# Performance work log

Measured on AMD Instinct MI355X. Metric: run time of the kernel, lower is better.

## Reference

```python
import jax, jax.numpy as jnp
import numpy as np

HEADS = 8
DIM_HEAD = 64
NB_FEATURES = 266
EPS = 1e-4


def softmax_kernel(data, projection, is_query):
    # data: (b, h, n, d); projection: (m, d)
    dn = data.shape[-1] ** -0.25                       # data normalizer d^{-1/4}
    ratio = projection.shape[0] ** -0.5                # m^{-1/2}
    dd = jnp.einsum('bhnd,md->bhnm', dn * data, projection)
    diag = (jnp.sum(data * data, axis=-1, keepdims=True) * 0.5) * (dn * dn)
    stab = jnp.max(dd, axis=-1, keepdims=True) if is_query else jnp.max(dd)
    return ratio * (jnp.exp(dd - diag - stab) + EPS)


def linear_attention(q, k, v):
    # q,k: (b,h,n,m) kernel features; v: (b,h,n,d)
    k_sum = k.sum(axis=-2)                                   # (b,h,m)
    D_inv = 1.0 / jnp.einsum('bhnm,bhm->bhn', q, k_sum)      # (b,h,n)
    context = jnp.einsum('bhnm,bhnd->bhmd', k, v)            # (b,h,m,d)
    return jnp.einsum('bhmd,bhnm,bhn->bhnd', context, q, D_inv)


def reference(x, W_qkv, W_out, projection, f):
    B, N, dim = x.shape
    h, dh = HEADS, DIM_HEAD
    qkv = x @ W_qkv                                          # (B,N,3*h*dh)
    q, k, v = jnp.split(qkv, 3, axis=-1)
    to_bh = lambda t: t.reshape(B, N, h, dh).transpose(0, 2, 1, 3).reshape(B * h, N, dh)
    q, k, v = to_bh(q), to_bh(k), to_bh(v)
    q = q * (dh ** -0.5)
    cls_q, q_ = q[:, :1], q[:, 1:]
    cls_k, k_ = k[:, :1], k[:, 1:]
    cls_v, v_ = v[:, :1], v[:, 1:]
    # cls token attends to ALL tokens with exact softmax attention
    sim = jnp.einsum('bid,bjd->bij', cls_q, k)
    cls_out = jnp.einsum('bij,bjd->bid', jax.nn.softmax(sim, axis=-1), v)
    # space attention regroup: 'b (f n) d -> (b f) n d'
    n_sp = (N - 1) // f
    grp = lambda t: t.reshape(B * h * f, n_sp, dh)
    q_, k_, v_ = grp(q_), grp(k_), grp(v_)
    # broadcast cls k/v to each group: 'b () d -> (b r) () d', r = f
    k_ = jnp.concatenate([jnp.repeat(cls_k, f, axis=0), k_], axis=1)  # (B*h*f, n_sp+1, dh)
    v_ = jnp.concatenate([jnp.repeat(cls_v, f, axis=0), v_], axis=1)
    # '(b h) f d -> b h f d'
    sh = lambda t: t.reshape(-1, h, t.shape[1], dh)
    qp = softmax_kernel(sh(q_), projection, True)
    kp = softmax_kernel(sh(k_), projection, False)
    out = linear_attention(qp, kp, sh(v_))                   # (-1, h, n_sp, dh)
    out = out.reshape(B * h, f * n_sp, dh)                   # '(b f) n d -> b (f n) d'
    out = jnp.concatenate([cls_out, out], axis=1)            # (B*h, N, dh)
    out = out.reshape(B, h, N, dh).transpose(0, 2, 1, 3).reshape(B, N, h * dh)
    return out @ W_out


def setup_inputs():
    key = jax.random.key(0)
    ks = jax.random.split(key, 3)
    B, F, S, dim = 8, 16, 196, 512
    N = 1 + F * S
    dh, m = DIM_HEAD, NB_FEATURES
    x = jax.random.normal(ks[0], (B, N, dim), dtype=jnp.float32)
    W_qkv = jax.random.normal(ks[1], (dim, 3 * dim), dtype=jnp.float32) * (dim ** -0.5)
    W_out = jax.random.normal(ks[2], (dim, dim), dtype=jnp.float32) * (dim ** -0.5)
    # gaussian orthogonal random matrix (scaling=0): QR blocks, chi-norm row scales
    rng = np.random.default_rng(0)
    blocks = []
    for _ in range(m // dh):
        qm, _ = np.linalg.qr(rng.standard_normal((dh, dh)))
        blocks.append(qm.T)
    rem = m - (m // dh) * dh
    if rem > 0:
        qm, _ = np.linalg.qr(rng.standard_normal((dh, dh)))
        blocks.append(qm.T[:rem])
    proj = np.concatenate(blocks, axis=0)
    multiplier = np.linalg.norm(rng.standard_normal((m, dh)), axis=1)
    projection = jnp.asarray(multiplier[:, None] * proj, dtype=jnp.float32)
    return {"x": x, "W_qkv": W_qkv, "W_out": W_out, "projection": projection, "f": F}
```

## Files before the change

kernel.cpp:

```cpp
#include <hip/hip_runtime.h>
#include <hip/hip_bf16.h>

namespace {

typedef __bf16 bf16x8 __attribute__((ext_vector_type(8)));
typedef float  f32x4  __attribute__((ext_vector_type(4)));
typedef unsigned short ushort8 __attribute__((ext_vector_type(8)));
typedef unsigned int u32;

constexpr int NTOK  = 3137;
constexpr int NH    = 8;
constexpr int DH    = 64;
constexpr int BH    = 64;
constexpr int MROWS = 8 * NTOK;
constexpr int NROWS = BH * NTOK;
constexpr int MF    = 266;
constexpr int MPK   = 320;
constexpr int MC    = 288;
constexpr int MS    = 320;
constexpr int NMAXB = (NROWS + 255) / 256;
constexpr int NCH   = 13;
constexpr int NBQKV = 197 * 12;
constexpr int NBOUT = 197 * 4;

constexpr float DN     = 0.35355339059327379f;
constexpr float HDN2   = 0.0625f;
constexpr float RATIO  = 0.0613139368f;
constexpr float EPSV   = 1.0e-4f;
constexpr float QSCALE = 0.125f;

__device__ __forceinline__ int swz64(int r, int c)  { return (r << 6) + (c ^ ((r & 7) << 3)); }
__device__ __forceinline__ int swz320(int r, int c) { return r * 320 + (c ^ ((r & 7) << 3)); }

__device__ __forceinline__ int xcdchunk(int bid, int nb) {
  const int q = nb >> 3, r = nb & 7;
  const int xcd = bid & 7, slot = bid >> 3;
  return (xcd < r ? xcd * (q + 1) : r * (q + 1) + (xcd - r) * q) + slot;
}

__device__ __forceinline__ float b2f(unsigned short u) {
  union { unsigned int i; float f; } cv;
  cv.i = ((unsigned int)u) << 16;
  return cv.f;
}
__device__ __forceinline__ unsigned short f2b(float f) {
  __hip_bfloat16 h = __float2bfloat16(f);
  union { __hip_bfloat16 h; unsigned short u; } cv;
  cv.h = h;
  return cv.u;
}
__device__ __forceinline__ unsigned int pk2(float a, float b) {
  return (unsigned int)f2b(a) | ((unsigned int)f2b(b) << 16);
}
__device__ __forceinline__ u32 fenc(float f) {
  u32 u = __float_as_uint(f);
  return (u & 0x80000000u) ? ~u : (u | 0x80000000u);
}
__device__ __forceinline__ float fdec(u32 u) {
  return __uint_as_float((u & 0x80000000u) ? (u ^ 0x80000000u) : ~u);
}
__device__ __forceinline__ void gload16(const void* g, void* l) {
  __builtin_amdgcn_global_load_lds(
      (const __attribute__((address_space(1))) u32*)g,
      (__attribute__((address_space(3))) u32*)l, 16, 0, 0);
}

__global__ __launch_bounds__(256) void k_projb(
    const float* __restrict__ proj, unsigned short* __restrict__ projb,
    u32* __restrict__ gmaxu)
{
  const int idx = (blockIdx.x * 256 + threadIdx.x) * 8;
  if (idx < MPK * 64) {
    const int m = idx >> 6, c0 = idx & 63;
    uint4 u;
    if (m < MF) {
      const float* src = proj + (size_t)m * 64 + c0;
      const float4 f0 = *(const float4*)src;
      const float4 f1 = *(const float4*)(src + 4);
      u.x = pk2(f0.x, f0.y); u.y = pk2(f0.z, f0.w);
      u.z = pk2(f1.x, f1.y); u.w = pk2(f1.z, f1.w);
    } else {
      u = uint4{0, 0, 0, 0};
    }
    *(uint4*)&projb[swz64(m, c0)] = u;
  }
  if (blockIdx.x == 0 && threadIdx.x == 0) *gmaxu = 0u;
}

__global__ __launch_bounds__(256) void k_cvt(
    const float* __restrict__ src, unsigned short* __restrict__ dst, int n8)
{
  const int i = blockIdx.x * 256 + threadIdx.x;
  if (i < n8) {
    const float4 f0 = *(const float4*)(src + (size_t)i * 8);
    const float4 f1 = *(const float4*)(src + (size_t)i * 8 + 4);
    uint4 u;
    u.x = pk2(f0.x, f0.y); u.y = pk2(f0.z, f0.w);
    u.z = pk2(f1.x, f1.y); u.w = pk2(f1.z, f1.w);
    *(uint4*)(dst + (size_t)i * 8) = u;
  }
}

__global__ __launch_bounds__(256) void k_tconv(
    const float* __restrict__ src, unsigned short* __restrict__ dst,
    int R, int C)
{
  __shared__ float tile[64][65];
  const int cb = blockIdx.x * 64, rb = blockIdx.y * 64;
  const int tid = threadIdx.x;
  const int tr = tid >> 4, tc4 = (tid & 15) * 4;
  #pragma unroll
  for (int i = 0; i < 4; ++i) {
    const int r = tr + i * 16;
    const float4 f = *(const float4*)(src + (size_t)(rb + r) * C + cb + tc4);
    tile[r][tc4 + 0] = f.x; tile[r][tc4 + 1] = f.y;
    tile[r][tc4 + 2] = f.z; tile[r][tc4 + 3] = f.w;
  }
  __syncthreads();
  #pragma unroll
  for (int i = 0; i < 4; ++i) {
    const int wrow = tr + i * 16;
    uint2 u;
    u.x = pk2(tile[tc4 + 0][wrow], tile[tc4 + 1][wrow]);
    u.y = pk2(tile[tc4 + 2][wrow], tile[tc4 + 3][wrow]);
    *(uint2*)&dst[(size_t)(cb + wrow) * R + rb + tc4] = u;
  }
}

__global__ __launch_bounds__(256) void k_qkv(
    const unsigned short* __restrict__ xb,
    const unsigned short* __restrict__ wT,
    unsigned short* __restrict__ qb, unsigned short* __restrict__ kb,
    unsigned short* __restrict__ vb)
{
  __shared__ alignas(16) unsigned short As[128 * 64];
  __shared__ alignas(16) unsigned short Bs[128 * 64];
  const int lid = xcdchunk(blockIdx.x, NBQKV);
  const int bm = lid / 12, bn = lid % 12;
  const int tid = threadIdx.x;
  const int lane = tid & 63, wid = tid >> 6;
  const int wr = wid >> 1, wc = wid & 1;
  const int row0 = bm * 128, col0 = bn * 128;
  const int l15 = lane & 15, l4 = lane >> 4;
  const int lr = lane >> 3;
  const int srcChunk = (lane & 7) ^ lr;

  const unsigned short* aRow[4];
  const unsigned short* bRow[4];
  #pragma unroll
  for (int j = 0; j < 4; ++j) {
    int gr = row0 + wid * 32 + j * 8 + lr;
    if (gr >= MROWS) gr = MROWS - 1;
    aRow[j] = xb + (size_t)gr * 512 + srcChunk * 8;
    bRow[j] = wT + (size_t)(col0 + wid * 32 + j * 8 + lr) * 512 + srcChunk * 8;
  }

  f32x4 acc[4][4];
  #pragma unroll
  for (int i = 0; i < 4; ++i)
    #pragma unroll
    for (int j = 0; j < 4; ++j) acc[i][j] = f32x4{0.f, 0.f, 0.f, 0.f};

  for (int kt = 0; kt < 512; kt += 64) {
    #pragma unroll
    for (int j = 0; j < 4; ++j) {
      gload16(aRow[j] + kt, &As[(wid * 32 + j * 8) * 64]);
      gload16(bRow[j] + kt, &Bs[(wid * 32 + j * 8) * 64]);
    }
    __syncthreads();
    #pragma unroll
    for (int ks = 0; ks < 2; ++ks) {
      bf16x8 af[4], bfr[4];
      #pragma unroll
      for (int i = 0; i < 4; ++i)
        af[i] = *(const bf16x8*)&As[swz64(wr * 64 + i * 16 + l15, ks * 32 + l4 * 8)];
      #pragma unroll
      for (int i = 0; i < 4; ++i)
        bfr[i] = *(const bf16x8*)&Bs[swz64(wc * 64 + i * 16 + l15, ks * 32 + l4 * 8)];
      #pragma unroll
      for (int mi = 0; mi < 4; ++mi)
        #pragma unroll
        for (int ni = 0; ni < 4; ++ni)
          acc[mi][ni] = __builtin_amdgcn_mfma_f32_16x16x32_bf16(
              af[mi], bfr[ni], acc[mi][ni], 0, 0, 0);
    }
    __syncthreads();
  }
  #pragma unroll
  for (int mi = 0; mi < 4; ++mi) {
    #pragma unroll
    for (int r = 0; r < 4; ++r) {
      const int grow = row0 + wr * 64 + mi * 16 + l4 * 4 + r;
      if (grow < MROWS) {
        const int bb = grow / NTOK, n = grow - bb * NTOK;
        #pragma unroll
        for (int ni = 0; ni < 4; ++ni) {
          const int gc = col0 + wc * 64 + ni * 16 + l15;
          const int which = gc >> 9;
          const int col = gc & 511;
          const int hh = col >> 6, d = col & 63;
          const size_t off = (size_t)((bb * NH + hh) * NTOK + n) * DH + d;
          const float vv = acc[mi][ni][r];
          if (which == 0)      qb[off] = f2b(vv * QSCALE);
          else if (which == 1) kb[off] = f2b(vv);
          else                 vb[off] = f2b(vv);
        }
      }
    }
  }
}

__global__ __launch_bounds__(256) void k_out(
    const unsigned short* __restrict__ a,
    const unsigned short* __restrict__ wT,
    float* __restrict__ out)
{
  __shared__ alignas(16) unsigned short As[128 * 64];
  __shared__ alignas(16) unsigned short Bs[128 * 64];
  const int lid = xcdchunk(blockIdx.x, NBOUT);
  const int bm = lid / 4, bn = lid % 4;
  const int tid = threadIdx.x;
  const int lane = tid & 63, wid = tid >> 6;
  const int wr = wid >> 1, wc = wid & 1;
  const int row0 = bm * 128, col0 = bn * 128;
  const int l15 = lane & 15, l4 = lane >> 4;
  const int lr = lane >> 3;
  const int srcChunk = (lane & 7) ^ lr;

  const unsigned short* aRow[4];
  const unsigned short* bRow[4];
  #pragma unroll
  for (int j = 0; j < 4; ++j) {
    int gr = row0 + wid * 32 + j * 8 + lr;
    if (gr >= MROWS) gr = MROWS - 1;
    aRow[j] = a + (size_t)gr * 512 + srcChunk * 8;
    bRow[j] = wT + (size_t)(col0 + wid * 32 + j * 8 + lr) * 512 + srcChunk * 8;
  }

  f32x4 acc[4][4];
  #pragma unroll
  for (int i = 0; i < 4; ++i)
    #pragma unroll
    for (int j = 0; j < 4; ++j) acc[i][j] = f32x4{0.f, 0.f, 0.f, 0.f};

  for (int kt = 0; kt < 512; kt += 64) {
    #pragma unroll
    for (int j = 0; j < 4; ++j) {
      gload16(aRow[j] + kt, &As[(wid * 32 + j * 8) * 64]);
      gload16(bRow[j] + kt, &Bs[(wid * 32 + j * 8) * 64]);
    }
    __syncthreads();
    #pragma unroll
    for (int ks = 0; ks < 2; ++ks) {
      bf16x8 af[4], bfr[4];
      #pragma unroll
      for (int i = 0; i < 4; ++i)
        af[i] = *(const bf16x8*)&As[swz64(wr * 64 + i * 16 + l15, ks * 32 + l4 * 8)];
      #pragma unroll
      for (int i = 0; i < 4; ++i)
        bfr[i] = *(const bf16x8*)&Bs[swz64(wc * 64 + i * 16 + l15, ks * 32 + l4 * 8)];
      #pragma unroll
      for (int mi = 0; mi < 4; ++mi)
        #pragma unroll
        for (int ni = 0; ni < 4; ++ni)
          acc[mi][ni] = __builtin_amdgcn_mfma_f32_16x16x32_bf16(
              af[mi], bfr[ni], acc[mi][ni], 0, 0, 0);
    }
    __syncthreads();
  }
  #pragma unroll
  for (int mi = 0; mi < 4; ++mi) {
    #pragma unroll
    for (int r = 0; r < 4; ++r) {
      const int grow = row0 + wr * 64 + mi * 16 + l4 * 4 + r;
      if (grow < MROWS) {
        #pragma unroll
        for (int ni = 0; ni < 4; ++ni) {
          const int gc = col0 + wc * 64 + ni * 16 + l15;
          out[(size_t)grow * 512 + gc] = acc[mi][ni][r];
        }
      }
    }
  }
}

__global__ __launch_bounds__(256) void k_cls1(
    const unsigned short* __restrict__ qb, const unsigned short* __restrict__ kb,
    float* __restrict__ simb, float* __restrict__ cmax)
{
  __shared__ float qv[64];
  __shared__ float sred[4];
  const int bh = blockIdx.x, ch = blockIdx.y, tid = threadIdx.x;
  if (tid < 64) qv[tid] = b2f(qb[(size_t)bh * NTOK * 64 + tid]);
  __syncthreads();
  const int j = ch * 256 + tid;
  float dot = -3e38f;
  if (j < NTOK) {
    const unsigned short* kr = kb + (size_t)bh * NTOK * 64 + (size_t)j * 64;
    dot = 0.f;
    #pragma unroll
    for (int d0 = 0; d0 < 64; d0 += 8) {
      const bf16x8 kv = *(const bf16x8*)(kr + d0);
      #pragma unroll
      for (int j2 = 0; j2 < 8; ++j2) dot += qv[d0 + j2] * (float)kv[j2];
    }
    simb[bh * 3200 + j] = dot;
  }
  float lm = dot;
  #pragma unroll
  for (int off = 32; off; off >>= 1) lm = fmaxf(lm, __shfl_xor(lm, off));
  if ((tid & 63) == 0) sred[tid >> 6] = lm;
  __syncthreads();
  if (tid == 0)
    cmax[bh * NCH + ch] = fmaxf(fmaxf(sred[0], sred[1]), fmaxf(sred[2], sred[3]));
}

__global__ __launch_bounds__(256) void k_cls2(
    const unsigned short* __restrict__ vb, const float* __restrict__ simb,
    const float* __restrict__ cmax, float* __restrict__ pacc,
    float* __restrict__ psum)
{
  __shared__ float pa[4][64];
  __shared__ float pw[4];
  const int bh = blockIdx.x, ch = blockIdx.y, tid = threadIdx.x;
  const int wave = tid >> 6, d = tid & 63;
  float mx = -3e38f;
  #pragma unroll
  for (int i = 0; i < NCH; ++i) mx = fmaxf(mx, cmax[bh * NCH + i]);
  float acc = 0.f, ps = 0.f;
  const int j0 = ch * 256 + wave * 64;
  for (int i = 0; i < 64; ++i) {
    const int j = j0 + i;
    if (j < NTOK) {
      const float p = __expf(simb[bh * 3200 + j] - mx);
      acc += p * b2f(vb[(size_t)bh * NTOK * 64 + (size_t)j * 64 + d]);
      ps += p;
    }
  }
  pa[wave][d] = acc;
  if (d == 0) pw[wave] = ps;
  __syncthreads();
  if (tid < 64)
    pacc[((size_t)bh * NCH + ch) * 64 + tid] = pa[0][tid] + pa[1][tid] + pa[2][tid] + pa[3][tid];
  if (tid == 0)
    psum[bh * NCH + ch] = pw[0] + pw[1] + pw[2] + pw[3];
}

__global__ __launch_bounds__(64) void k_cls3(
    const float* __restrict__ pacc, const float* __restrict__ psum,
    unsigned short* __restrict__ attnb)
{
  const int bh = blockIdx.x, d = threadIdx.x;
  float a = 0.f, s = 0.f;
  #pragma unroll
  for (int ch = 0; ch < NCH; ++ch) {
    a += pacc[((size_t)bh * NCH + ch) * 64 + d];
    s += psum[bh * NCH + ch];
  }
  const int bb = bh >> 3, hh = bh & 7;
  attnb[((size_t)bb * NTOK + 0) * 512 + hh * 64 + d] = f2b(a / s);
}

__global__ __launch_bounds__(256) void k_keymax(
    const unsigned short* __restrict__ kb, const unsigned short* __restrict__ projb,
    u32* __restrict__ gmaxu)
{
  __shared__ alignas(16) unsigned short projL[MPK * 64];
  __shared__ float red[4];
  const int blk = blockIdx.x, tid = threadIdx.x;
  const int lane = tid & 63, wave = tid >> 6;
  const int l15 = lane & 15, l4 = lane >> 4;
  const int mw0 = wave * 80;
  {
    const char* srcb = (const char*)projb;
    char* dstb = (char*)projL;
    #pragma unroll
    for (int j = 0; j < 10; ++j) {
      const int off = (j * 4 + wave) * 1024;
      gload16(srcb + off + lane * 16, dstb + off);
    }
  }
  __syncthreads();
  float lm = -3e38f;
  for (int rg = 0; rg < 4; ++rg) {
    const int row0 = (blk * 4 + rg) * 64;
    if (row0 >= NROWS) break;
    bf16x8 bfrag[4][2];
    #pragma unroll
    for (int tf = 0; tf < 4; ++tf) {
      int gr = row0 + tf * 16 + l15;
      if (gr >= NROWS) gr = NROWS - 1;
      #pragma unroll
      for (int ks = 0; ks < 2; ++ks)
        bfrag[tf][ks] = *(const bf16x8*)(kb + (size_t)gr * 64 + ks * 32 + l4 * 8);
    }
    f32x4 acc[5][4];
    #pragma unroll
    for (int i = 0; i < 5; ++i)
      #pragma unroll
      for (int j = 0; j < 4; ++j) acc[i][j] = f32x4{0.f, 0.f, 0.f, 0.f};
    #pragma unroll
    for (int mf = 0; mf < 5; ++mf) {
      const bf16x8 a0 = *(const bf16x8*)&projL[swz64(mw0 + mf * 16 + l15, l4 * 8)];
      const bf16x8 a1 = *(const bf16x8*)&projL[swz64(mw0 + mf * 16 + l15, 32 + l4 * 8)];
      #pragma unroll
      for (int tf = 0; tf < 4; ++tf) {
        acc[mf][tf] = __builtin_amdgcn_mfma_f32_16x16x32_bf16(a0, bfrag[tf][0], acc[mf][tf], 0, 0, 0);
        acc[mf][tf] = __builtin_amdgcn_mfma_f32_16x16x32_bf16(a1, bfrag[tf][1], acc[mf][tf], 0, 0, 0);
      }
    }
    #pragma unroll
    for (int tf = 0; tf < 4; ++tf) {
      const bool colok = (row0 + tf * 16 + l15) < NROWS;
      #pragma unroll
      for (int mf = 0; mf < 5; ++mf)
        #pragma unroll
        for (int r = 0; r < 4; ++r) {
          const int m = mw0 + mf * 16 + l4 * 4 + r;
          if (colok && m < MF) lm = fmaxf(lm, DN * acc[mf][tf][r]);
        }
    }
  }
  #pragma unroll
  for (int off = 32; off; off >>= 1) lm = fmaxf(lm, __shfl_xor(lm, off));
  if (lane == 0) red[wave] = lm;
  __syncthreads();
  if (tid == 0) {
    const float bm = fmaxf(fmaxf(red[0], red[1]), fmaxf(red[2], red[3]));
    atomicMax(gmaxu, fenc(bm));
  }
}

__global__ __launch_bounds__(512) void k_ctx(
    const unsigned short* __restrict__ kb, const unsigned short* __restrict__ vb,
    const unsigned short* __restrict__ projb, const u32* __restrict__ gmaxu,
    unsigned short* __restrict__ ctxg, float* __restrict__ ksumg)
{
  __shared__ alignas(16) unsigned short kpT[MC * 64];
  __shared__ alignas(16) unsigned short vT[64 * 64];
  __shared__ float diag_l[64];

  const int g = blockIdx.x, bh = g >> 4, c = g & 15;
  const int tid = threadIdx.x;
  const int lane = tid & 63, wave = tid >> 6;
  const int l15 = lane & 15, l4 = lane >> 4;
  const int nf = (wave < 2) ? 3 : 2;
  const int M0 = (wave < 2) ? wave * 48 : 96 + (wave - 2) * 32;
  const float gm = fdec(*gmaxu);

  bf16x8 pfr[3][2];
  #pragma unroll
  for (int mf = 0; mf < 3; ++mf)
    #pragma unroll
    for (int ks = 0; ks < 2; ++ks)
      pfr[mf][ks] = (mf < nf)
          ? *(const bf16x8*)&projb[swz64(M0 + mf * 16 + l15, ks * 32 + l4 * 8)]
          : bf16x8{0, 0, 0, 0, 0, 0, 0, 0};

  const unsigned short* ksrc = kb + (size_t)bh * NTOK * 64;
  const unsigned short* vsrc = vb + (size_t)bh * NTOK * 64;

  f32x4 ctxacc[3][4];
  #pragma unroll
  for (int i = 0; i < 3; ++i)
    #pragma unroll
    for (int j = 0; j < 4; ++j) ctxacc[i][j] = f32x4{0.f, 0.f, 0.f, 0.f};
  float ksump[3][4];
  #pragma unroll
  for (int i = 0; i < 3; ++i)
    #pragma unroll
    for (int j = 0; j < 4; ++j) ksump[i][j] = 0.f;

  for (int kt = 0; kt < 4; ++kt) {
    __syncthreads();
    {
      const int t = tid & 63, dblk = (tid >> 6) & 7;
      const int n = kt * 64 + t;
      if (n < 197) {
        const int node = (n == 0) ? 0 : 1 + c * 196 + (n - 1);
        const ushort8 v = *(const ushort8*)(vsrc + (size_t)node * 64 + dblk * 8);
        #pragma unroll
        for (int j = 0; j < 8; ++j) vT[swz64(dblk * 8 + j, t)] = v[j];
      } else {
        #pragma unroll
        for (int j = 0; j < 8; ++j) vT[swz64(dblk * 8 + j, t)] = 0;
      }
    }
    if (tid < 64) {
      const int n = kt * 64 + tid;
      const int nn = (n < 197) ? n : 0;
      const int node = (nn == 0) ? 0 : 1 + c * 196 + (nn - 1);
      const unsigned short* kr = ksrc + (size_t)node * 64;
      float s = 0.f;
      #pragma unroll
      for (int d0 = 0; d0 < 64; d0 += 8) {
        const bf16x8 v = *(const bf16x8*)(kr + d0);
        #pragma unroll
        for (int j = 0; j < 8; ++j) { const float f = (float)v[j]; s += f * f; }
      }
      diag_l[tid] = HDN2 * s;
    }
    __syncthreads();
    #pragma unroll
    for (int tf = 0; tf < 4; ++tf) {
      const int n = kt * 64 + tf * 16 + l15;
      const int nn = (n < 197) ? n : 0;
      const int node = (nn == 0) ? 0 : 1 + c * 196 + (nn - 1);
      bf16x8 b0 = *(const bf16x8*)(ksrc + (size_t)node * 64 + l4 * 8);
      bf16x8 b1 = *(const bf16x8*)(ksrc + (size_t)node * 64 + 32 + l4 * 8);
      f32x4 a1[3];
      #pragma unroll
      for (int mf = 0; mf < 3; ++mf) {
        a1[mf] = f32x4{0.f, 0.f, 0.f, 0.f};
        if (mf < nf) {
          a1[mf] = __builtin_amdgcn_mfma_f32_16x16x32_bf16(pfr[mf][0], b0, a1[mf], 0, 0, 0);
          a1[mf] = __builtin_amdgcn_mfma_f32_16x16x32_bf16(pfr[mf][1], b1, a1[mf], 0, 0, 0);
        }
      }
      const int t = tf * 16 + l15;
      const int nv = kt * 64 + t;
      const float dg = diag_l[t];
      #pragma unroll
      for (int mf = 0; mf < 3; ++mf) {
        if (mf < nf) {
          #pragma unroll
          for (int r = 0; r < 4; ++r) {
            const int m = M0 + mf * 16 + l4 * 4 + r;
            float kp = 0.f;
            if (m < MF && nv < 197)
              kp = RATIO * (__expf(DN * a1[mf][r] - dg - gm) + EPSV);
            ksump[mf][r] += kp;
            kpT[swz64(m, t)] = f2b(kp);
          }
        }
      }
    }
    #pragma unroll
    for (int ks = 0; ks < 2; ++ks) {
      bf16x8 a2[3];
      #pragma unroll
      for (int mf = 0; mf < 3; ++mf)
        if (mf < nf)
          a2[mf] = *(const bf16x8*)&kpT[swz64(M0 + mf * 16 + l15, ks * 32 + l4 * 8)];
      #pragma unroll
      for (int df = 0; df < 4; ++df) {
        const bf16x8 b2 = *(const bf16x8*)&vT[swz64(df * 16 + l15, ks * 32 + l4 * 8)];
        #pragma unroll
        for (int mf = 0; mf < 3; ++mf)
          if (mf < nf)
            ctxacc[mf][df] = __builtin_amdgcn_mfma_f32_16x16x32_bf16(a2[mf], b2, ctxacc[mf][df], 0, 0, 0);
      }
    }
  }
  #pragma unroll
  for (int mf = 0; mf < 3; ++mf) {
    if (mf < nf) {
      #pragma unroll
      for (int r = 0; r < 4; ++r) {
        float v = ksump[mf][r];
        v += __shfl_xor(v, 1); v += __shfl_xor(v, 2);
        v += __shfl_xor(v, 4); v += __shfl_xor(v, 8);
        if (l15 == 0) ksumg[(size_t)g * MC + M0 + mf * 16 + l4 * 4 + r] = v;
      }
    }
  }
  #pragma unroll
  for (int mf = 0; mf < 3; ++mf) {
    if (mf < nf) {
      #pragma unroll
      for (int df = 0; df < 4; ++df) {
        const int d = df * 16 + l15;
        const int m = M0 + mf * 16 + l4 * 4;
        uint2 u;
        u.x = pk2(ctxacc[mf][df][0], ctxacc[mf][df][1]);
        u.y = pk2(ctxacc[mf][df][2], ctxacc[mf][df][3]);
        *(uint2*)&ctxg[(size_t)g * 64 * MS + swz320(d, m)] = u;
      }
    }
  }
}

__global__ __launch_bounds__(512) void k_qry(
    const unsigned short* __restrict__ qb, const unsigned short* __restrict__ projb,
    const unsigned short* __restrict__ ctxg, const float* __restrict__ ksumg,
    unsigned short* __restrict__ attnb)
{
  __shared__ alignas(16) unsigned short qp[64 * 320];
  __shared__ alignas(16) unsigned short ctxL[64 * 320];
  __shared__ float diag_l[64];
  __shared__ float rmax_l[8][64];
  __shared__ float dnm_l[8][64];

  const int g = blockIdx.x, bh = g >> 4, c = g & 15;
  const int bb = bh >> 3, hh = bh & 7;
  const int tid = threadIdx.x;
  const int lane = tid & 63, wave = tid >> 6;
  const int l15 = lane & 15, l4 = lane >> 4;
  const int nf = (wave < 2) ? 3 : 2;
  const int M0 = (wave < 2) ? wave * 48 : 96 + (wave - 2) * 32;

  {
    const char* srcb = (const char*)(ctxg + (size_t)g * 64 * MS);
    char* dstb = (char*)ctxL;
    #pragma unroll
    for (int j = 0; j < 5; ++j) {
      const int off = (j * 8 + wave) * 1024;
      gload16(srcb + off + lane * 16, dstb + off);
    }
  }

  bf16x8 pfr[3][2];
  #pragma unroll
  for (int mf = 0; mf < 3; ++mf)
    #pragma unroll
    for (int ks = 0; ks < 2; ++ks)
      pfr[mf][ks] = (mf < nf)
          ? *(const bf16x8*)&projb[swz64(M0 + mf * 16 + l15, ks * 32 + l4 * 8)]
          : bf16x8{0, 0, 0, 0, 0, 0, 0, 0};

  float ksr[3][4];
  #pragma unroll
  for (int mf = 0; mf < 3; ++mf) {
    if (mf < nf) {
      const float4 kv = *(const float4*)(ksumg + (size_t)g * MC + M0 + mf * 16 + l4 * 4);
      ksr[mf][0] = kv.x; ksr[mf][1] = kv.y; ksr[mf][2] = kv.z; ksr[mf][3] = kv.w;
    } else {
      ksr[mf][0] = ksr[mf][1] = ksr[mf][2] = ksr[mf][3] = 0.f;
    }
  }

  const unsigned short* qsrc = qb + (size_t)bh * NTOK * 64;
  const int tf4 = wave & 3, dfh = wave >> 2;

  for (int qt = 0; qt < 4; ++qt) {
    __syncthreads();
    if (tid < 64) {
      const int n = qt * 64 + tid;
      const int nn = (n < 196) ? n : 0;
      const int node = 1 + c * 196 + nn;
      const unsigned short* qr = qsrc + (size_t)node * 64;
      float s = 0.f;
      #pragma unroll
      for (int d0 = 0; d0 < 64; d0 += 8) {
        const bf16x8 v = *(const bf16x8*)(qr + d0);
        #pragma unroll
        for (int j = 0; j < 8; ++j) { const float f = (float)v[j]; s += f * f; }
      }
      diag_l[tid] = HDN2 * s;
    }
    f32x4 acc3[3][4];
    #pragma unroll
    for (int i = 0; i < 3; ++i)
      #pragma unroll
      for (int j = 0; j < 4; ++j) acc3[i][j] = f32x4{0.f, 0.f, 0.f, 0.f};
    #pragma unroll
    for (int tf = 0; tf < 4; ++tf) {
      const int n = qt * 64 + tf * 16 + l15;
      const int nn = (n < 196) ? n : 0;
      const int node = 1 + c * 196 + nn;
      bf16x8 b0 = *(const bf16x8*)(qsrc + (size_t)node * 64 + l4 * 8);
      bf16x8 b1 = *(const bf16x8*)(qsrc + (size_t)node * 64 + 32 + l4 * 8);
      #pragma unroll
      for (int mf = 0; mf < 3; ++mf) {
        if (mf < nf) {
          acc3[mf][tf] = __builtin_amdgcn_mfma_f32_16x16x32_bf16(pfr[mf][0], b0, acc3[mf][tf], 0, 0, 0);
          acc3[mf][tf] = __builtin_amdgcn_mfma_f32_16x16x32_bf16(pfr[mf][1], b1, acc3[mf][tf], 0, 0, 0);
        }
      }
    }
    #pragma unroll
    for (int tf = 0; tf < 4; ++tf) {
      float v = -3e38f;
      #pragma unroll
      for (int mf = 0; mf < 3; ++mf)
        if (mf < nf)
          #pragma unroll
          for (int r = 0; r < 4; ++r) {
            const int m = M0 + mf * 16 + l4 * 4 + r;
            if (m < MF) v = fmaxf(v, DN * acc3[mf][tf][r]);
          }
      v = fmaxf(v, __shfl_xor(v, 16));
      v = fmaxf(v, __shfl_xor(v, 32));
      if (l4 == 0) rmax_l[wave][tf * 16 + l15] = v;
    }
    __syncthreads();
    #pragma unroll
    for (int tf = 0; tf < 4; ++tf) {
      const int t = tf * 16 + l15;
      const int tq = qt * 64 + t;
      float rm = fmaxf(fmaxf(rmax_l[0][t], rmax_l[1][t]), fmaxf(rmax_l[2][t], rmax_l[3][t]));
      rm = fmaxf(rm, fmaxf(fmaxf(rmax_l[4][t], rmax_l[5][t]), fmaxf(rmax_l[6][t], rmax_l[7][t])));
      const float dg = diag_l[t];
      float dpart = 0.f;
      #pragma unroll
      for (int mf = 0; mf < 3; ++mf) {
        if (mf < nf) {
          float e[4];
          #pragma unroll
          for (int r = 0; r < 4; ++r) {
            const int m = M0 + mf * 16 + l4 * 4 + r;
            e[r] = (m < MF && tq < 196)
                 ? RATIO * (__expf(DN * acc3[mf][tf][r] - dg - rm) + EPSV) : 0.f;
            dpart += e[r] * ksr[mf][r];
          }
          uint2 u; u.x = pk2(e[0], e[1]); u.y = pk2(e[2], e[3]);
          *(uint2*)&qp[swz320(t, M0 + mf * 16 + l4 * 4)] = u;
        }
      }
      dpart += __shfl_xor(dpart, 16);
      dpart += __shfl_xor(dpart, 32);
      if (l4 == 0) dnm_l[wave][t] = dpart;
    }
    __syncthreads();
    f32x4 oacc[2];
    oacc[0] = f32x4{0.f, 0.f, 0.f, 0.f};
    oacc[1] = f32x4{0.f, 0.f, 0.f, 0.f};
    #pragma unroll
    for (int ks = 0; ks < 9; ++ks) {
      const bf16x8 a4 = *(const bf16x8*)&qp[swz320(tf4 * 16 + l15, ks * 32 + l4 * 8)];
      #pragma unroll
      for (int di = 0; di < 2; ++di) {
        const int d = dfh * 32 + di * 16 + l15;
        const bf16x8 b4 = *(const bf16x8*)&ctxL[swz320(d, ks * 32 + l4 * 8)];
        oacc[di] = __builtin_amdgcn_mfma_f32_16x16x32_bf16(a4, b4, oacc[di], 0, 0, 0);
      }
    }
    #pragma unroll
    for (int r = 0; r < 4; ++r) {
      const int tl = tf4 * 16 + l4 * 4 + r;
      const int tq = qt * 64 + tl;
      if (tq < 196) {
        float denom = 0.f;
        #pragma unroll
        for (int w8 = 0; w8 < 8; ++w8) denom += dnm_l[w8][tl];
        const float dinv = 1.0f / denom;
        const int node = 1 + c * 196 + tq;
        unsigned short* orow = attnb + ((size_t)bb * NTOK + node) * 512 + hh * 64 + dfh * 32;
        #pragma unroll
        for (int di = 0; di < 2; ++di)
          orow[di * 16 + l15] = f2b(oacc[di][r] * dinv);
      }
    }
  }
}

}

extern "C" void kernel_launch(void* const* d_in, const int* in_sizes, int n_in,
                              void* d_out, int out_size, void* d_ws, size_t ws_size,
                              hipStream_t stream) {
  (void)in_sizes; (void)n_in; (void)out_size; (void)ws_size;
  const float* x    = (const float*)d_in[0];
  const float* wqkv = (const float*)d_in[1];
  const float* wout = (const float*)d_in[2];
  const float* proj = (const float*)d_in[3];
  float* out = (float*)d_out;

  const size_t QKV = (size_t)BH * NTOK * DH;
  unsigned short* qb    = (unsigned short*)d_ws;
  unsigned short* kb    = qb + QKV;
  unsigned short* vb    = kb + QKV;
  unsigned short* attnb = vb + QKV;
  float* fbase = (float*)(attnb + QKV);
  u32*   gmaxu = (u32*)(fbase + 4096);
  float* simb = fbase + 8192;
  float* cmax = simb + 64 * 3200;
  float* pacc = cmax + 1024;
  float* psum = pacc + 64 * NCH * 64;
  unsigned short* wqkvT = (unsigned short*)(psum + 1024);
  unsigned short* woutT = wqkvT + 1536 * 512;
  unsigned short* ctxg  = woutT + 512 * 512;
  float* ksumg = (float*)(ctxg + (size_t)1024 * 64 * MS);
  unsigned short* projb = (unsigned short*)(ksumg + 1024 * MC);
  unsigned short* xb = attnb;

  const dim3 blk(256);
  k_projb  <<<dim3(10),       blk, 0, stream>>>(proj, projb, gmaxu);
  k_tconv  <<<dim3(24, 8),    blk, 0, stream>>>(wqkv, wqkvT, 512, 1536);
  k_tconv  <<<dim3(8, 8),     blk, 0, stream>>>(wout, woutT, 512, 512);
  k_cvt    <<<dim3((int)(QKV / 8 + 255) / 256), blk, 0, stream>>>(x, xb, (int)(QKV / 8));
  k_qkv    <<<dim3(NBQKV),    blk, 0, stream>>>(xb, wqkvT, qb, kb, vb);
  k_cls1   <<<dim3(BH, NCH),  blk, 0, stream>>>(qb, kb, simb, cmax);
  k_cls2   <<<dim3(BH, NCH),  blk, 0, stream>>>(vb, simb, cmax, pacc, psum);
  k_cls3   <<<dim3(BH), dim3(64), 0, stream>>>(pacc, psum, attnb);
  k_keymax <<<dim3(NMAXB),    blk, 0, stream>>>(kb, projb, gmaxu);
  k_ctx    <<<dim3(1024), dim3(512), 0, stream>>>(kb, vb, projb, gmaxu, ctxg, ksumg);
  k_qry    <<<dim3(1024), dim3(512), 0, stream>>>(qb, projb, ctxg, ksumg, attnb);
  k_out    <<<dim3(NBOUT),    blk, 0, stream>>>(attnb, woutT, out);
}
```

Baseline: 354.8 us.

## Software-pipeline query tiles in k_qry with double-buffered LDS

Splits the per-tile query loop into stages (diag, feature MFMA plus row max, exp/qp write, output MFMA). The output MFMA for the previous tile now runs alongside the feature MFMA for the current tile, using double-buffered qp, diag, rmax and dnm arrays in LDS. This removes one barrier per iteration and lets the two matrix phases interleave. In exchange the kernel uses roughly 40KB more LDS, which may reduce how many blocks fit on each CU.

```diff
diff --git a/kernel.cpp b/kernel.cpp
--- a/kernel.cpp
+++ b/kernel.cpp
@@ -585,11 +585,11 @@
     const unsigned short* __restrict__ ctxg, const float* __restrict__ ksumg,
     unsigned short* __restrict__ attnb)
 {
-  __shared__ alignas(16) unsigned short qp[64 * 320];
+  __shared__ alignas(16) unsigned short qp[2][64 * 320];
   __shared__ alignas(16) unsigned short ctxL[64 * 320];
-  __shared__ float diag_l[64];
-  __shared__ float rmax_l[8][64];
-  __shared__ float dnm_l[8][64];
+  __shared__ float diag_l[2][64];
+  __shared__ float rmax_l[2][8][64];
+  __shared__ float dnm_l[2][8][64];
 
   const int g = blockIdx.x, bh = g >> 4, c = g & 15;
   const int bb = bh >> 3, hh = bh & 7;
@@ -632,8 +632,7 @@
   const unsigned short* qsrc = qb + (size_t)bh * NTOK * 64;
   const int tf4 = wave & 3, dfh = wave >> 2;
 
-  for (int qt = 0; qt < 4; ++qt) {
-    __syncthreads();
+  auto diagf = [&](int qt, int buf) {
     if (tid < 64) {
       const int n = qt * 64 + tid;
       const int nn = (n < 196) ? n : 0;
@@ -646,9 +645,10 @@
         #pragma unroll
         for (int j = 0; j < 8; ++j) { const float f = (float)v[j]; s += f * f; }
       }
-      diag_l[tid] = HDN2 * s;
-    }
-    f32x4 acc3[3][4];
+      diag_l[buf][tid] = HDN2 * s;
+    }
+  };
+  auto stage3f = [&](int qt, int buf, f32x4 (&acc3)[3][4]) {
     #pragma unroll
     for (int i = 0; i < 3; ++i)
       #pragma unroll
@@ -681,16 +681,19 @@
           }
       v = fmaxf(v, __shfl_xor(v, 16));
       v = fmaxf(v, __shfl_xor(v, 32));
-      if (l4 == 0) rmax_l[wave][tf * 16 + l15] = v;
-    }
-    __syncthreads();
+      if (l4 == 0) rmax_l[buf][wave][tf * 16 + l15] = v;
+    }
+  };
+  auto qpwritef = [&](int qt, int buf, const f32x4 (&acc3)[3][4]) {
     #pragma unroll
     for (int tf = 0; tf < 4; ++tf) {
       const int t = tf * 16 + l15;
       const int tq = qt * 64 + t;
-      float rm = fmaxf(fmaxf(rmax_l[0][t], rmax_l[1][t]), fmaxf(rmax_l[2][t], rmax_l[3][t]));
-      rm = fmaxf(rm, fmaxf(fmaxf(rmax_l[4][t], rmax_l[5][t]), fmaxf(rmax_l[6][t], rmax_l[7][t])));
-      const float dg = diag_l[t];
+      float rm = fmaxf(fmaxf(rmax_l[buf][0][t], rmax_l[buf][1][t]),
+                       fmaxf(rmax_l[buf][2][t], rmax_l[buf][3][t]));
+      rm = fmaxf(rm, fmaxf(fmaxf(rmax_l[buf][4][t], rmax_l[buf][5][t]),
+                           fmaxf(rmax_l[buf][6][t], rmax_l[buf][7][t])));
+      const float dg = diag_l[buf][t];
       float dpart = 0.f;
       #pragma unroll
       for (int mf = 0; mf < 3; ++mf) {
@@ -704,20 +707,21 @@
             dpart += e[r] * ksr[mf][r];
           }
           uint2 u; u.x = pk2(e[0], e[1]); u.y = pk2(e[2], e[3]);
-          *(uint2*)&qp[swz320(t, M0 + mf * 16 + l4 * 4)] = u;
+          *(uint2*)&qp[buf][swz320(t, M0 + mf * 16 + l4 * 4)] = u;
         }
       }
       dpart += __shfl_xor(dpart, 16);
       dpart += __shfl_xor(dpart, 32);
-      if (l4 == 0) dnm_l[wave][t] = dpart;
-    }
-    __syncthreads();
+      if (l4 == 0) dnm_l[buf][wave][t] = dpart;
+    }
+  };
+  auto stage4f = [&](int qt, int buf) {
     f32x4 oacc[2];
     oacc[0] = f32x4{0.f, 0.f, 0.f, 0.f};
     oacc[1] = f32x4{0.f, 0.f, 0.f, 0.f};
     #pragma unroll
     for (int ks = 0; ks < 9; ++ks) {
-      const bf16x8 a4 = *(const bf16x8*)&qp[swz320(tf4 * 16 + l15, ks * 32 + l4 * 8)];
+      const bf16x8 a4 = *(const bf16x8*)&qp[buf][swz320(tf4 * 16 + l15, ks * 32 + l4 * 8)];
       #pragma unroll
       for (int di = 0; di < 2; ++di) {
         const int d = dfh * 32 + di * 16 + l15;
@@ -732,7 +736,7 @@
       if (tq < 196) {
         float denom = 0.f;
         #pragma unroll
-        for (int w8 = 0; w8 < 8; ++w8) denom += dnm_l[w8][tl];
+        for (int w8 = 0; w8 < 8; ++w8) denom += dnm_l[buf][w8][tl];
         const float dinv = 1.0f / denom;
         const int node = 1 + c * 196 + tq;
         unsigned short* orow = attnb + ((size_t)bb * NTOK + node) * 512 + hh * 64 + dfh * 32;
@@ -741,7 +745,24 @@
           orow[di * 16 + l15] = f2b(oacc[di][r] * dinv);
       }
     }
-  }
+  };
+
+  f32x4 acc3[3][4];
+  diagf(0, 0);
+  stage3f(0, 0, acc3);
+  __syncthreads();
+  qpwritef(0, 0, acc3);
+  for (int qt = 1; qt < 4; ++qt) {
+    const int b = qt & 1, pb = b ^ 1;
+    __syncthreads();
+    diagf(qt, b);
+    stage4f(qt - 1, pb);
+    stage3f(qt, b, acc3);
+    __syncthreads();
+    qpwritef(qt, b, acc3);
+  }
+  __syncthreads();
+  stage4f(3, 1);
 }
 
 }
```

After: 344.8 us. 1.03x faster.
